# Performance work log

Measured on AMD Instinct MI355X. Metric: run time of the kernel, lower is better.

## Reference

```python
import jax, jax.numpy as jnp
import numpy as np
from jax import lax

B, N, T, H, C = 131072, 62, 5, 32, 3


def lstm(x, w_ih, w_hh, b_ih, b_hh):
    # x: (B, T, I); gates order i,f,g,o (PyTorch convention)
    b, t, _ = x.shape
    h_dim = w_hh.shape[1]
    xg = jnp.einsum('bti,gi->btg', x, w_ih) + b_ih + b_hh  # (B,T,4H)

    def step(carry, xg_t):
        h, c = carry
        g = xg_t + h @ w_hh.T
        i, f, gg, o = jnp.split(g, 4, axis=-1)
        c = jax.nn.sigmoid(f) * c + jax.nn.sigmoid(i) * jnp.tanh(gg)
        h = jax.nn.sigmoid(o) * jnp.tanh(c)
        return (h, c), h

    z = jnp.zeros((b, h_dim), dtype=x.dtype)
    _, hs = lax.scan(step, (z, z), xg.transpose(1, 0, 2))
    return hs.transpose(1, 0, 2)  # (B,T,H)


def ln_lrelu(x, g, b):
    # LayerNorm over last two dims (seq_len, hidden) jointly, then LeakyReLU(0.01)
    mu = x.mean(axis=(1, 2), keepdims=True)
    var = x.var(axis=(1, 2), keepdims=True)
    y = (x - mu) * lax.rsqrt(var + 1e-5) * g + b
    return jax.nn.leaky_relu(y, 0.01)


def setup_inputs() -> dict:
    key = jax.random.key(0)
    ks = jax.random.split(key, 16)
    sc = lambda fan: 1.0 / np.sqrt(H)
    d = {
        'data': jax.random.normal(ks[0], (B, 1, N, T), dtype=jnp.float32),
        'w_ih0': jax.random.uniform(ks[1], (4 * H, N), minval=-sc(N), maxval=sc(N)),
        'w_hh0': jax.random.uniform(ks[2], (4 * H, H), minval=-sc(H), maxval=sc(H)),
        'b_ih0': jax.random.uniform(ks[3], (4 * H,), minval=-sc(H), maxval=sc(H)),
        'b_hh0': jax.random.uniform(ks[4], (4 * H,), minval=-sc(H), maxval=sc(H)),
        'g0': jnp.ones((T, H), jnp.float32),
        'be0': jnp.zeros((T, H), jnp.float32),
        'w_ih1': jax.random.uniform(ks[5], (4 * H, H), minval=-sc(H), maxval=sc(H)),
        'w_hh1': jax.random.uniform(ks[6], (4 * H, H), minval=-sc(H), maxval=sc(H)),
        'b_ih1': jax.random.uniform(ks[7], (4 * H,), minval=-sc(H), maxval=sc(H)),
        'b_hh1': jax.random.uniform(ks[8], (4 * H,), minval=-sc(H), maxval=sc(H)),
        'g1': jnp.ones((T, H), jnp.float32),
        'be1': jnp.zeros((T, H), jnp.float32),
        'dw': jax.random.normal(ks[9], (C, T * H), dtype=jnp.float32) * 0.05,
        'db': jnp.zeros((C,), jnp.float32),
    }
    return d


def reference(data, w_ih0, w_hh0, b_ih0, b_hh0, g0, be0,
              w_ih1, w_hh1, b_ih1, b_hh1, g1, be1, dw, db):
    x = data.squeeze(1).transpose(0, 2, 1)  # (B, T, N)
    out0 = ln_lrelu(lstm(x, w_ih0, w_hh0, b_ih0, b_hh0), g0, be0)   # dropout=eval
    out1 = ln_lrelu(lstm(out0, w_ih1, w_hh1, b_ih1, b_hh1), g1, be1)
    out = out1 + out0  # residual
    flat = out.reshape(out.shape[0], -1)  # (B, T*H)
    return jax.nn.leaky_relu(flat @ dw.T + db, 0.01)
```

## Files before the change

### kernel.cpp

```cpp
#include <hip/hip_runtime.h>

#define THREADS 256
#define SPB 4

__device__ __forceinline__ float frcp(float x){ return __builtin_amdgcn_rcpf(x); }
__device__ __forceinline__ float fsig(float x){ return frcp(1.0f + __expf(-x)); }
__device__ __forceinline__ float ftanh(float x){
    float e = __expf(2.0f * x);
    return fmaf(-2.0f, frcp(e + 1.0f), 1.0f);
}
__device__ __forceinline__ float lrelu(float x){ return x > 0.0f ? x : 0.01f * x; }

__global__ void diag_kernel(float* outp, float code){ outp[0] = code; }

__device__ __forceinline__ void lstm_rec_fw(const float* __restrict__ whh,
                                            const float (&acc)[5][2],
                                            float* __restrict__ hout,
                                            int lane, int j, int p,
                                            float& s1o, float& s2o)
{
    float wh0[32], wh1[32];
    {
        const float* r0 = whh + (size_t)((2*p + 0)*32 + j)*32;
        const float* r1 = whh + (size_t)((2*p + 1)*32 + j)*32;
        #pragma unroll
        for (int q = 0; q < 8; ++q){
            float4 a = *(const float4*)(r0 + q*4);
            wh0[q*4+0]=a.x; wh0[q*4+1]=a.y; wh0[q*4+2]=a.z; wh0[q*4+3]=a.w;
            float4 b = *(const float4*)(r1 + q*4);
            wh1[q*4+0]=b.x; wh1[q*4+1]=b.y; wh1[q*4+2]=b.z; wh1[q*4+3]=b.w;
        }
    }
    const bool lo = (lane < 32);
    const float sc  = p ? 2.0f : -1.0f;
    float h = 0.0f, c = 0.0f, s1 = 0.0f, s2 = 0.0f;
    #pragma unroll
    for (int t = 0; t < 5; ++t){
        float q0a = acc[t][0], q1 = acc[t][1], q0b = 0.0f, q1b = 0.0f;
        if (t > 0){
            const float* hp = hout + (t-1)*32;
            #pragma unroll
            for (int k0 = 0; k0 < 32; k0 += 8){
                float4 ha = *(const float4*)(hp + k0);
                float4 hc = *(const float4*)(hp + k0 + 4);
                q0a = fmaf(wh0[k0+0], ha.x, q0a);  q1  = fmaf(wh1[k0+0], ha.x, q1);
                q0a = fmaf(wh0[k0+1], ha.y, q0a);  q1  = fmaf(wh1[k0+1], ha.y, q1);
                q0a = fmaf(wh0[k0+2], ha.z, q0a);  q1  = fmaf(wh1[k0+2], ha.z, q1);
                q0a = fmaf(wh0[k0+3], ha.w, q0a);  q1  = fmaf(wh1[k0+3], ha.w, q1);
                q0b = fmaf(wh0[k0+4], hc.x, q0b);  q1b = fmaf(wh1[k0+4], hc.x, q1b);
                q0b = fmaf(wh0[k0+5], hc.y, q0b);  q1b = fmaf(wh1[k0+5], hc.y, q1b);
                q0b = fmaf(wh0[k0+6], hc.z, q0b);  q1b = fmaf(wh1[k0+6], hc.z, q1b);
                q0b = fmaf(wh0[k0+7], hc.w, q0b);  q1b = fmaf(wh1[k0+7], hc.w, q1b);
            }
        }
        float q0 = q0a + q0b;
        float qf = q1 + q1b;
        float v0;
        if (p == 0) v0 = fsig(q0);
        else        v0 = fmaf(2.0f, fsig(2.0f*q0), -1.0f);
        float v1 = fsig(qf);
        float x0 = __shfl_xor(v0, 32, 64);
        float x1 = __shfl_xor(v1, 32, 64);
        float iv = p ? x0 : v0;
        float gv = p ? v0 : x0;
        float fv = p ? x1 : v1;
        float ov = p ? v1 : x1;
        c = fmaf(fv, c, iv * gv);
        h = ov * ftanh(c);
        s1 += h; s2 = fmaf(h, h, s2);
        if (lo) hout[t*32 + j] = h;
    }
    (void)sc;
    s1o = s1; s2o = s2;
}

__global__ __launch_bounds__(THREADS, 1)
void reslstm_kernel(const float* __restrict__ data,
                    const float* __restrict__ wih0, const float* __restrict__ whh0,
                    const float* __restrict__ bih0, const float* __restrict__ bhh0,
                    const float* __restrict__ g0p,  const float* __restrict__ be0p,
                    const float* __restrict__ wih1, const float* __restrict__ whh1,
                    const float* __restrict__ bih1, const float* __restrict__ bhh1,
                    const float* __restrict__ g1p,  const float* __restrict__ be1p,
                    const float* __restrict__ dwp,  const float* __restrict__ dbp,
                    float* __restrict__ outp, int Btot)
{
    __shared__ __attribute__((aligned(16))) float xs[SPB*320];
    __shared__ __attribute__((aligned(16))) float wbuf[128*68];
    __shared__ __attribute__((aligned(16))) float out0s[SPB*160];
    __shared__ float bias0s[128], bias1s[128];
    __shared__ float g0s[160], be0s[160], g1s[160], be1s[160];
    __shared__ float dws[480];
    __shared__ float dbs[3];

    const int tid = threadIdx.x;
    const int b0  = blockIdx.x * SPB;
    const int nsamp = (Btot - b0 < SPB) ? (Btot - b0) : SPB;

    {
        const float* dat = data + (size_t)b0 * 310;
        for (int i = tid; i < nsamp*310; i += THREADS){
            int s = i / 310, r = i - s*310;
            int n = r / 5,   t = r - n*5;
            xs[s*320 + t*64 + n] = dat[i];
        }
        for (int i = tid; i < SPB*10; i += THREADS){
            int s = i / 10, q = i - s*10;
            xs[s*320 + (q>>1)*64 + 62 + (q&1)] = 0.0f;
        }
        for (int i = tid; i < 128*62; i += THREADS){
            int row = i / 62, n = i - row*62;
            wbuf[row*68 + n] = wih0[i];
        }
        for (int i = tid; i < 128*6; i += THREADS){
            int row = i / 6, n = i - row*6;
            wbuf[row*68 + 62 + n] = 0.0f;
        }
        if (tid < 128)  bias0s[tid] = bih0[tid] + bhh0[tid];
        else            { int q = tid - 128; bias1s[q] = bih1[q] + bhh1[q]; }
        if (tid < 160){
            g0s[tid] = g0p[tid];  be0s[tid] = be0p[tid];
            g1s[tid] = g1p[tid];  be1s[tid] = be1p[tid];
        }
        for (int i = tid; i < 480; i += THREADS) dws[i] = dwp[i];
        if (tid < 3) dbs[tid] = dbp[tid];
    }
    __syncthreads();

    const int lane = tid & 63;
    const int j    = lane & 31;
    const int p    = lane >> 5;
    const int s    = tid >> 6;
    const bool lo  = (lane < 32);

    float* xsc  = xs    + s*320;
    float* o0l  = out0s + s*160;

    float acc[5][2];
    {
        float bv0 = bias0s[(2*p + 0)*32 + j];
        float bv1 = bias0s[(2*p + 1)*32 + j];
        #pragma unroll
        for (int t = 0; t < 5; ++t){ acc[t][0] = bv0; acc[t][1] = bv1; }
    }
    {
        const float* wp = wbuf + (size_t)(64*p + j)*68;
        #pragma unroll 4
        for (int n0 = 0; n0 < 64; n0 += 4){
            float4 w0 = *(const float4*)(wp + n0);
            float4 w1 = *(const float4*)(wp + 32*68 + n0);
            #pragma unroll
            for (int t = 0; t < 5; ++t){
                float4 xv = *(const float4*)(xsc + t*64 + n0);
                acc[t][0] = fmaf(w0.x, xv.x, fmaf(w0.y, xv.y, fmaf(w0.z, xv.z, fmaf(w0.w, xv.w, acc[t][0]))));
                acc[t][1] = fmaf(w1.x, xv.x, fmaf(w1.y, xv.y, fmaf(w1.z, xv.z, fmaf(w1.w, xv.w, acc[t][1]))));
            }
        }
    }

    {
        float s1, s2;
        lstm_rec_fw(whh0, acc, o0l, lane, j, p, s1, s2);
        #pragma unroll
        for (int m = 1; m <= 32; m <<= 1){
            s1 += __shfl_xor(s1, m, 64);
            s2 += __shfl_xor(s2, m, 64);
        }
        float mu   = s1 * (1.0f/320.0f);
        float var  = s2 * (1.0f/320.0f) - mu*mu;
        float rstd = rsqrtf(var + 1e-5f);
        #pragma unroll
        for (int t = 0; t < 5; ++t){
            float v = o0l[t*32 + j];
            float y = lrelu(fmaf((v - mu)*rstd, g0s[t*32 + j], be0s[t*32 + j]));
            if (lo) o0l[t*32 + j] = y;
        }
    }

    __syncthreads();
    for (int i = tid; i < 128*32; i += THREADS){
        int row = i >> 5, k = i & 31;
        wbuf[row*36 + k] = wih1[i];
    }
    for (int i = tid; i < 128*4; i += THREADS){
        int row = i >> 2;
        wbuf[row*36 + 32 + (i & 3)] = 0.0f;
    }
    __syncthreads();

    {
        float bv0 = bias1s[(2*p + 0)*32 + j];
        float bv1 = bias1s[(2*p + 1)*32 + j];
        #pragma unroll
        for (int t = 0; t < 5; ++t){ acc[t][0] = bv0; acc[t][1] = bv1; }
    }
    {
        const float* wp1 = wbuf + (size_t)(64*p + j)*36;
        #pragma unroll 4
        for (int k0 = 0; k0 < 32; k0 += 4){
            float4 w0 = *(const float4*)(wp1 + k0);
            float4 w1 = *(const float4*)(wp1 + 32*36 + k0);
            #pragma unroll
            for (int t = 0; t < 5; ++t){
                float4 ov = *(const float4*)(o0l + t*32 + k0);
                acc[t][0] = fmaf(w0.x, ov.x, fmaf(w0.y, ov.y, fmaf(w0.z, ov.z, fmaf(w0.w, ov.w, acc[t][0]))));
                acc[t][1] = fmaf(w1.x, ov.x, fmaf(w1.y, ov.y, fmaf(w1.z, ov.z, fmaf(w1.w, ov.w, acc[t][1]))));
            }
        }
    }

    float p0 = 0.0f, p1 = 0.0f, p2 = 0.0f;
    {
        float s1, s2;
        lstm_rec_fw(whh1, acc, xsc, lane, j, p, s1, s2);
        #pragma unroll
        for (int m = 1; m <= 32; m <<= 1){
            s1 += __shfl_xor(s1, m, 64);
            s2 += __shfl_xor(s2, m, 64);
        }
        float mu   = s1 * (1.0f/320.0f);
        float var  = s2 * (1.0f/320.0f) - mu*mu;
        float rstd = rsqrtf(var + 1e-5f);
        #pragma unroll
        for (int t = 0; t < 5; ++t){
            float v  = xsc[t*32 + j];
            float y  = lrelu(fmaf((v - mu)*rstd, g1s[t*32 + j], be1s[t*32 + j]));
            float o  = y + o0l[t*32 + j];
            p0 = fmaf(dws[      t*32 + j], o, p0);
            p1 = fmaf(dws[160 + t*32 + j], o, p1);
            p2 = fmaf(dws[320 + t*32 + j], o, p2);
        }
    }
    #pragma unroll
    for (int m = 1; m <= 32; m <<= 1){
        p0 += __shfl_xor(p0, m, 64);
        p1 += __shfl_xor(p1, m, 64);
        p2 += __shfl_xor(p2, m, 64);
    }
    if (lane < 3 && s < nsamp){
        float v = (lane == 0) ? p0 : ((lane == 1) ? p1 : p2);
        v = lrelu(fmaf(0.5f, v, dbs[lane]));
        outp[(size_t)(b0 + s)*3 + lane] = v;
    }
}

extern "C" void kernel_launch(void* const* d_in, const int* in_sizes, int n_in,
                              void* d_out, int out_size, void* d_ws, size_t ws_size,
                              hipStream_t stream)
{
    (void)d_ws; (void)ws_size;

    const int B = out_size / 3;

    int idx_data = 0;
    for (int i = 1; i < n_in; ++i)
        if (in_sizes[i] > in_sizes[idx_data]) idx_data = i;

    static const int dict_map[15]  = {0,1,2,3,4,5,6,7,8,9,10,11,12,13,14};
    static const int alpha_map[15] = {6,13,11,2,0,9,4,14,12,3,1,10,5,8,7};
    static const int rev_map[15]   = {14,13,12,11,10,9,8,7,6,5,4,3,2,1,0};

    const int* map = dict_map;
    if (idx_data == 6)       map = alpha_map;
    else if (idx_data == 14) map = rev_map;

    long ds  = (long)in_sizes[idx_data];
    long ws0 = (long)in_sizes[map[1]];
    bool ok = (ds == (long)B*310 || ds == (long)B*620 || ds == (long)B*1240)
           && (ws0 == 7936 || ws0 == 15872 || ws0 == 31744);

    if (!ok || B <= 0){
        diag_kernel<<<1, 1, 0, stream>>>((float*)d_out, 100.0f + 10.0f*idx_data);
        return;
    }

    const float* P[15];
    for (int k = 0; k < 15; ++k) P[k] = (const float*)d_in[map[k]];

    const int nblocks = (B + SPB - 1) / SPB;
    reslstm_kernel<<<dim3(nblocks), dim3(THREADS), 0, stream>>>(
        P[0], P[1], P[2], P[3], P[4], P[5], P[6], P[7], P[8], P[9],
        P[10], P[11], P[12], P[13], P[14],
        (float*)d_out, B);
}
```

Baseline: 1.247 ms.

## Map one sample per block with one gate row per thread

Restructures the kernel so each 128-thread block handles a single sample. Each thread owns one of the 128 gate rows, and gate activations are exchanged through shared memory with block barriers at every timestep. It drops the LDS staging of input weights, biases and LayerNorm parameters, reading them straight from global memory instead. The aim is to cut per-thread register and shared-memory footprint and raise occupancy, at the cost of twice the threads per sample, per-step __syncthreads, and repeated per-block global weight reads.

```diff
diff --git a/kernel.cpp b/kernel.cpp
--- a/kernel.cpp
+++ b/kernel.cpp
@@ -1,7 +1,6 @@
 #include <hip/hip_runtime.h>
 
-#define THREADS 256
-#define SPB 4
+#define THREADS 128
 
 __device__ __forceinline__ float frcp(float x){ return __builtin_amdgcn_rcpf(x); }
 __device__ __forceinline__ float fsig(float x){ return frcp(1.0f + __expf(-x)); }
@@ -13,64 +12,49 @@
 
 __global__ void diag_kernel(float* outp, float code){ outp[0] = code; }
 
-__device__ __forceinline__ void lstm_rec_fw(const float* __restrict__ whh,
-                                            const float (&acc)[5][2],
-                                            float* __restrict__ hout,
-                                            int lane, int j, int p,
-                                            float& s1o, float& s2o)
+__device__ __forceinline__ void lstm_layer(const float* __restrict__ whh_row,
+                                           float (&acc)[5],
+                                           float* __restrict__ hout,
+                                           float* __restrict__ abuf,
+                                           int g, int j,
+                                           float ak, float aa, float ab,
+                                           float& s1o, float& s2o)
 {
-    float wh0[32], wh1[32];
-    {
-        const float* r0 = whh + (size_t)((2*p + 0)*32 + j)*32;
-        const float* r1 = whh + (size_t)((2*p + 1)*32 + j)*32;
-        #pragma unroll
-        for (int q = 0; q < 8; ++q){
-            float4 a = *(const float4*)(r0 + q*4);
-            wh0[q*4+0]=a.x; wh0[q*4+1]=a.y; wh0[q*4+2]=a.z; wh0[q*4+3]=a.w;
-            float4 b = *(const float4*)(r1 + q*4);
-            wh1[q*4+0]=b.x; wh1[q*4+1]=b.y; wh1[q*4+2]=b.z; wh1[q*4+3]=b.w;
-        }
-    }
-    const bool lo = (lane < 32);
-    const float sc  = p ? 2.0f : -1.0f;
-    float h = 0.0f, c = 0.0f, s1 = 0.0f, s2 = 0.0f;
+    float wh[32];
+    #pragma unroll
+    for (int q = 0; q < 8; ++q){
+        float4 v = *(const float4*)(whh_row + q*4);
+        wh[q*4+0]=v.x; wh[q*4+1]=v.y; wh[q*4+2]=v.z; wh[q*4+3]=v.w;
+    }
+    float c = 0.0f, s1 = 0.0f, s2 = 0.0f;
     #pragma unroll
     for (int t = 0; t < 5; ++t){
-        float q0a = acc[t][0], q1 = acc[t][1], q0b = 0.0f, q1b = 0.0f;
+        float qa = acc[t], qb = 0.0f, qc = 0.0f, qd = 0.0f;
         if (t > 0){
             const float* hp = hout + (t-1)*32;
             #pragma unroll
             for (int k0 = 0; k0 < 32; k0 += 8){
-                float4 ha = *(const float4*)(hp + k0);
-                float4 hc = *(const float4*)(hp + k0 + 4);
-                q0a = fmaf(wh0[k0+0], ha.x, q0a);  q1  = fmaf(wh1[k0+0], ha.x, q1);
-                q0a = fmaf(wh0[k0+1], ha.y, q0a);  q1  = fmaf(wh1[k0+1], ha.y, q1);
-                q0a = fmaf(wh0[k0+2], ha.z, q0a);  q1  = fmaf(wh1[k0+2], ha.z, q1);
-                q0a = fmaf(wh0[k0+3], ha.w, q0a);  q1  = fmaf(wh1[k0+3], ha.w, q1);
-                q0b = fmaf(wh0[k0+4], hc.x, q0b);  q1b = fmaf(wh1[k0+4], hc.x, q1b);
-                q0b = fmaf(wh0[k0+5], hc.y, q0b);  q1b = fmaf(wh1[k0+5], hc.y, q1b);
-                q0b = fmaf(wh0[k0+6], hc.z, q0b);  q1b = fmaf(wh1[k0+6], hc.z, q1b);
-                q0b = fmaf(wh0[k0+7], hc.w, q0b);  q1b = fmaf(wh1[k0+7], hc.w, q1b);
-            }
-        }
-        float q0 = q0a + q0b;
-        float qf = q1 + q1b;
-        float v0;
-        if (p == 0) v0 = fsig(q0);
-        else        v0 = fmaf(2.0f, fsig(2.0f*q0), -1.0f);
-        float v1 = fsig(qf);
-        float x0 = __shfl_xor(v0, 32, 64);
-        float x1 = __shfl_xor(v1, 32, 64);
-        float iv = p ? x0 : v0;
-        float gv = p ? v0 : x0;
-        float fv = p ? x1 : v1;
-        float ov = p ? v1 : x1;
-        c = fmaf(fv, c, iv * gv);
-        h = ov * ftanh(c);
+                float4 h0 = *(const float4*)(hp + k0);
+                float4 h1 = *(const float4*)(hp + k0 + 4);
+                qa = fmaf(wh[k0+0], h0.x, qa);  qb = fmaf(wh[k0+1], h0.y, qb);
+                qc = fmaf(wh[k0+2], h0.z, qc);  qd = fmaf(wh[k0+3], h0.w, qd);
+                qa = fmaf(wh[k0+4], h1.x, qa);  qb = fmaf(wh[k0+5], h1.y, qb);
+                qc = fmaf(wh[k0+6], h1.z, qc);  qd = fmaf(wh[k0+7], h1.w, qd);
+            }
+        }
+        float qs = (qa + qb) + (qc + qd);
+        abuf[g] = fmaf(aa, fsig(ak * qs), ab);
+        __syncthreads();
+        float ai = abuf[     j];
+        float af = abuf[32 + j];
+        float ag = abuf[64 + j];
+        float ao = abuf[96 + j];
+        c = fmaf(af, c, ai * ag);
+        float h = ao * ftanh(c);
         s1 += h; s2 = fmaf(h, h, s2);
-        if (lo) hout[t*32 + j] = h;
-    }
-    (void)sc;
+        if (g < 32) hout[t*32 + j] = h;
+        __syncthreads();
+    }
     s1o = s1; s2o = s2;
 }
 
@@ -85,82 +69,57 @@
                     const float* __restrict__ dwp,  const float* __restrict__ dbp,
                     float* __restrict__ outp, int Btot)
 {
-    __shared__ __attribute__((aligned(16))) float xs[SPB*320];
-    __shared__ __attribute__((aligned(16))) float wbuf[128*68];
-    __shared__ __attribute__((aligned(16))) float out0s[SPB*160];
-    __shared__ float bias0s[128], bias1s[128];
-    __shared__ float g0s[160], be0s[160], g1s[160], be1s[160];
-    __shared__ float dws[480];
-    __shared__ float dbs[3];
+    __shared__ __attribute__((aligned(16))) float xs[320];
+    __shared__ __attribute__((aligned(16))) float obuf[160];
+    __shared__ __attribute__((aligned(16))) float abuf[128];
 
     const int tid = threadIdx.x;
-    const int b0  = blockIdx.x * SPB;
-    const int nsamp = (Btot - b0 < SPB) ? (Btot - b0) : SPB;
-
-    {
-        const float* dat = data + (size_t)b0 * 310;
-        for (int i = tid; i < nsamp*310; i += THREADS){
-            int s = i / 310, r = i - s*310;
-            int n = r / 5,   t = r - n*5;
-            xs[s*320 + t*64 + n] = dat[i];
-        }
-        for (int i = tid; i < SPB*10; i += THREADS){
-            int s = i / 10, q = i - s*10;
-            xs[s*320 + (q>>1)*64 + 62 + (q&1)] = 0.0f;
-        }
-        for (int i = tid; i < 128*62; i += THREADS){
-            int row = i / 62, n = i - row*62;
-            wbuf[row*68 + n] = wih0[i];
-        }
-        for (int i = tid; i < 128*6; i += THREADS){
-            int row = i / 6, n = i - row*6;
-            wbuf[row*68 + 62 + n] = 0.0f;
-        }
-        if (tid < 128)  bias0s[tid] = bih0[tid] + bhh0[tid];
-        else            { int q = tid - 128; bias1s[q] = bih1[q] + bhh1[q]; }
-        if (tid < 160){
-            g0s[tid] = g0p[tid];  be0s[tid] = be0p[tid];
-            g1s[tid] = g1p[tid];  be1s[tid] = be1p[tid];
-        }
-        for (int i = tid; i < 480; i += THREADS) dws[i] = dwp[i];
-        if (tid < 3) dbs[tid] = dbp[tid];
+    const int b   = blockIdx.x;
+    const int g   = tid;
+    const int j   = g & 31;
+    const bool isg = (g >= 64) && (g < 96);
+    const float ak = isg ? 2.0f : 1.0f;
+    const float aa = isg ? 2.0f : 1.0f;
+    const float ab = isg ? -1.0f : 0.0f;
+
+    {
+        const float* dat = data + (size_t)b * 310;
+        for (int i = tid; i < 310; i += THREADS){
+            int n = i / 5, t = i - n*5;
+            xs[t*64 + n] = dat[i];
+        }
+        if (tid < 10) xs[(tid>>1)*64 + 62 + (tid&1)] = 0.0f;
     }
     __syncthreads();
 
-    const int lane = tid & 63;
-    const int j    = lane & 31;
-    const int p    = lane >> 5;
-    const int s    = tid >> 6;
-    const bool lo  = (lane < 32);
-
-    float* xsc  = xs    + s*320;
-    float* o0l  = out0s + s*160;
-
-    float acc[5][2];
-    {
-        float bv0 = bias0s[(2*p + 0)*32 + j];
-        float bv1 = bias0s[(2*p + 1)*32 + j];
-        #pragma unroll
-        for (int t = 0; t < 5; ++t){ acc[t][0] = bv0; acc[t][1] = bv1; }
-    }
-    {
-        const float* wp = wbuf + (size_t)(64*p + j)*68;
-        #pragma unroll 4
-        for (int n0 = 0; n0 < 64; n0 += 4){
-            float4 w0 = *(const float4*)(wp + n0);
-            float4 w1 = *(const float4*)(wp + 32*68 + n0);
+    float acc[5];
+    {
+        float bv = bih0[g] + bhh0[g];
+        #pragma unroll
+        for (int t = 0; t < 5; ++t) acc[t] = bv;
+        const float* wr = wih0 + (size_t)g * 62;
+        #pragma unroll
+        for (int n0 = 0; n0 < 60; n0 += 4){
+            float2 wa = *(const float2*)(wr + n0);
+            float2 wb = *(const float2*)(wr + n0 + 2);
             #pragma unroll
             for (int t = 0; t < 5; ++t){
-                float4 xv = *(const float4*)(xsc + t*64 + n0);
-                acc[t][0] = fmaf(w0.x, xv.x, fmaf(w0.y, xv.y, fmaf(w0.z, xv.z, fmaf(w0.w, xv.w, acc[t][0]))));
-                acc[t][1] = fmaf(w1.x, xv.x, fmaf(w1.y, xv.y, fmaf(w1.z, xv.z, fmaf(w1.w, xv.w, acc[t][1]))));
-            }
+                float4 xv = *(const float4*)(xs + t*64 + n0);
+                acc[t] = fmaf(wa.x, xv.x, fmaf(wa.y, xv.y,
+                         fmaf(wb.x, xv.z, fmaf(wb.y, xv.w, acc[t]))));
+            }
+        }
+        float2 wt = *(const float2*)(wr + 60);
+        #pragma unroll
+        for (int t = 0; t < 5; ++t){
+            float2 xv = *(const float2*)(xs + t*64 + 60);
+            acc[t] = fmaf(wt.x, xv.x, fmaf(wt.y, xv.y, acc[t]));
         }
     }
 
     {
         float s1, s2;
-        lstm_rec_fw(whh0, acc, o0l, lane, j, p, s1, s2);
+        lstm_layer(whh0 + (size_t)g*32, acc, obuf, abuf, g, j, ak, aa, ab, s1, s2);
         #pragma unroll
         for (int m = 1; m <= 32; m <<= 1){
             s1 += __shfl_xor(s1, m, 64);
@@ -169,50 +128,38 @@
         float mu   = s1 * (1.0f/320.0f);
         float var  = s2 * (1.0f/320.0f) - mu*mu;
         float rstd = rsqrtf(var + 1e-5f);
-        #pragma unroll
-        for (int t = 0; t < 5; ++t){
-            float v = o0l[t*32 + j];
-            float y = lrelu(fmaf((v - mu)*rstd, g0s[t*32 + j], be0s[t*32 + j]));
-            if (lo) o0l[t*32 + j] = y;
-        }
-    }
-
+        {
+            float v = obuf[tid];
+            obuf[tid] = lrelu(fmaf((v - mu)*rstd, g0p[tid], be0p[tid]));
+            if (tid < 32){
+                float v2 = obuf[128 + tid];
+                obuf[128 + tid] = lrelu(fmaf((v2 - mu)*rstd, g0p[128 + tid], be0p[128 + tid]));
+            }
+        }
+    }
     __syncthreads();
-    for (int i = tid; i < 128*32; i += THREADS){
-        int row = i >> 5, k = i & 31;
-        wbuf[row*36 + k] = wih1[i];
-    }
-    for (int i = tid; i < 128*4; i += THREADS){
-        int row = i >> 2;
-        wbuf[row*36 + 32 + (i & 3)] = 0.0f;
-    }
-    __syncthreads();
-
-    {
-        float bv0 = bias1s[(2*p + 0)*32 + j];
-        float bv1 = bias1s[(2*p + 1)*32 + j];
-        #pragma unroll
-        for (int t = 0; t < 5; ++t){ acc[t][0] = bv0; acc[t][1] = bv1; }
-    }
-    {
-        const float* wp1 = wbuf + (size_t)(64*p + j)*36;
-        #pragma unroll 4
+
+    {
+        float bv = bih1[g] + bhh1[g];
+        #pragma unroll
+        for (int t = 0; t < 5; ++t) acc[t] = bv;
+        const float* wr = wih1 + (size_t)g * 32;
+        #pragma unroll
         for (int k0 = 0; k0 < 32; k0 += 4){
-            float4 w0 = *(const float4*)(wp1 + k0);
-            float4 w1 = *(const float4*)(wp1 + 32*36 + k0);
+            float4 w = *(const float4*)(wr + k0);
             #pragma unroll
             for (int t = 0; t < 5; ++t){
-                float4 ov = *(const float4*)(o0l + t*32 + k0);
-                acc[t][0] = fmaf(w0.x, ov.x, fmaf(w0.y, ov.y, fmaf(w0.z, ov.z, fmaf(w0.w, ov.w, acc[t][0]))));
-                acc[t][1] = fmaf(w1.x, ov.x, fmaf(w1.y, ov.y, fmaf(w1.z, ov.z, fmaf(w1.w, ov.w, acc[t][1]))));
-            }
-        }
-    }
-
-    float p0 = 0.0f, p1 = 0.0f, p2 = 0.0f;
+                float4 ov = *(const float4*)(obuf + t*32 + k0);
+                acc[t] = fmaf(w.x, ov.x, fmaf(w.y, ov.y,
+                         fmaf(w.z, ov.z, fmaf(w.w, ov.w, acc[t]))));
+            }
+        }
+    }
+
+    float* h1 = xs;
     {
         float s1, s2;
-        lstm_rec_fw(whh1, acc, xsc, lane, j, p, s1, s2);
+        lstm_layer(whh1 + (size_t)g*32, acc, h1, abuf, g, j, ak, aa, ab, s1, s2);
         #pragma unroll
         for (int m = 1; m <= 32; m <<= 1){
             s1 += __shfl_xor(s1, m, 64);
@@ -221,26 +168,39 @@
         float mu   = s1 * (1.0f/320.0f);
         float var  = s2 * (1.0f/320.0f) - mu*mu;
         float rstd = rsqrtf(var + 1e-5f);
+        {
+            float v = h1[tid];
+            h1[tid] = lrelu(fmaf((v - mu)*rstd, g1p[tid], be1p[tid])) + obuf[tid];
+            if (tid < 32){
+                float v2 = h1[128 + tid];
+                h1[128 + tid] = lrelu(fmaf((v2 - mu)*rstd, g1p[128 + tid], be1p[128 + tid]))
+                              + obuf[128 + tid];
+            }
+        }
+    }
+    __syncthreads();
+
+    if (g < 32){
+        float p0 = 0.0f, p1 = 0.0f, p2 = 0.0f;
         #pragma unroll
         for (int t = 0; t < 5; ++t){
-            float v  = xsc[t*32 + j];
-            float y  = lrelu(fmaf((v - mu)*rstd, g1s[t*32 + j], be1s[t*32 + j]));
-            float o  = y + o0l[t*32 + j];
-            p0 = fmaf(dws[      t*32 + j], o, p0);
-            p1 = fmaf(dws[160 + t*32 + j], o, p1);
-            p2 = fmaf(dws[320 + t*32 + j], o, p2);
-        }
-    }
-    #pragma unroll
-    for (int m = 1; m <= 32; m <<= 1){
-        p0 += __shfl_xor(p0, m, 64);
-        p1 += __shfl_xor(p1, m, 64);
-        p2 += __shfl_xor(p2, m, 64);
-    }
-    if (lane < 3 && s < nsamp){
-        float v = (lane == 0) ? p0 : ((lane == 1) ? p1 : p2);
-        v = lrelu(fmaf(0.5f, v, dbs[lane]));
-        outp[(size_t)(b0 + s)*3 + lane] = v;
+            float v = h1[t*32 + j];
+            p0 = fmaf(dwp[      t*32 + j], v, p0);
+            p1 = fmaf(dwp[160 + t*32 + j], v, p1);
+            p2 = fmaf(dwp[320 + t*32 + j], v, p2);
+        }
+        #pragma unroll
+        for (int m = 1; m <= 16; m <<= 1){
+            p0 += __shfl_xor(p0, m, 64);
+            p1 += __shfl_xor(p1, m, 64);
+            p2 += __shfl_xor(p2, m, 64);
+        }
+        if (j == 0){
+            size_t o = (size_t)b * 3;
+            outp[o + 0] = lrelu(p0 + dbp[0]);
+            outp[o + 1] = lrelu(p1 + dbp[1]);
+            outp[o + 2] = lrelu(p2 + dbp[2]);
+        }
     }
 }
 
@@ -277,8 +237,7 @@
     const float* P[15];
     for (int k = 0; k < 15; ++k) P[k] = (const float*)d_in[map[k]];
 
-    const int nblocks = (B + SPB - 1) / SPB;
-    reslstm_kernel<<<dim3(nblocks), dim3(THREADS), 0, stream>>>(
+    reslstm_kernel<<<dim3(B), dim3(THREADS), 0, stream>>>(
         P[0], P[1], P[2], P[3], P[4], P[5], P[6], P[7], P[8], P[9],
         P[10], P[11], P[12], P[13], P[14],
         (float*)d_out, B);
```

New measurement: 1.518 ms. +21.8%, slower.
